# Kernel tuning notes

Hardware: AMD Instinct MI355X
Metric: run time of the kernel (lower is better)

Reference implementation:

```python
import jax, jax.numpy as jnp
import numpy as np

B = 512
NV = 6890   # SMPL vertices
NJ = 24     # SMPL joints
NB = 10     # shape betas
NP = 207    # pose blend coeffs = 23*9
# canonical SMPL kinematic tree: parent of joints 1..23
PARENT = np.array([0, 0, 0, 1, 2, 3, 4, 5, 6, 7, 8, 9, 9, 9, 12, 13, 14, 16, 17, 18, 19, 20, 21], dtype=np.int64)


def quat2mat(quat):
    # quat: [N,4] (w,x,y,z) -> [N,3,3]
    q = quat / jnp.linalg.norm(quat, axis=1, keepdims=True)
    w, x, y, z = q[:, 0], q[:, 1], q[:, 2], q[:, 3]
    w2, x2, y2, z2 = w * w, x * x, y * y, z * z
    wx, wy, wz = w * x, w * y, w * z
    xy, xz, yz = x * y, x * z, y * z
    rot = jnp.stack([
        w2 + x2 - y2 - z2, 2 * xy - 2 * wz, 2 * wy + 2 * xz,
        2 * wz + 2 * xy, w2 - x2 + y2 - z2, 2 * yz - 2 * wx,
        2 * xz - 2 * wy, 2 * wx + 2 * yz, w2 - x2 - y2 + z2], axis=1)
    return rot.reshape(-1, 3, 3)


def rodrigues(theta):
    # theta: [N,3] axis-angle -> [N,3,3]
    angle = jnp.linalg.norm(theta + 1e-8, axis=1, keepdims=True)
    normalized = theta / angle
    half = angle * 0.5
    quat = jnp.concatenate([jnp.cos(half), jnp.sin(half) * normalized], axis=1)
    return quat2mat(quat)


def setup_inputs() -> dict:
    key = jax.random.key(0)
    ks = jax.random.split(key, 8)
    pose = jax.random.normal(ks[0], (B, NJ * 3), dtype=jnp.float32) * 0.2
    beta = jax.random.normal(ks[1], (B, NB), dtype=jnp.float32)
    v_template = jax.random.normal(ks[2], (NV, 3), dtype=jnp.float32)
    shapedirs = jax.random.normal(ks[3], (NV, 3, NB), dtype=jnp.float32) * 0.01
    posedirs = jax.random.normal(ks[4], (NV, 3, NP), dtype=jnp.float32) * 0.01
    Jr = jax.random.uniform(ks[5], (NJ, NV), dtype=jnp.float32)
    J_regressor = Jr / jnp.sum(Jr, axis=1, keepdims=True)
    W = jax.random.uniform(ks[6], (NV, NJ), dtype=jnp.float32)
    weights = W / jnp.sum(W, axis=1, keepdims=True)
    return {"pose": pose, "beta": beta, "v_template": v_template,
            "shapedirs": shapedirs, "posedirs": posedirs,
            "J_regressor": J_regressor, "weights": weights,
            "parent": PARENT}


def reference(pose, beta, v_template, shapedirs, posedirs, J_regressor, weights, parent):
    dt = pose.dtype
    bsz = pose.shape[0]
    # shape blend: v_shaped [B,V,3]
    v_shaped = jnp.einsum('vdk,bk->bvd', shapedirs, beta) + v_template[None]
    J = jnp.einsum('jv,bvd->bjd', J_regressor, v_shaped)  # [B,24,3]
    # per-joint rotations from axis-angle
    R = rodrigues(pose.reshape(-1, 3)).reshape(bsz, NJ, 3, 3)
    # pose blend
    I3 = jnp.eye(3, dtype=dt)
    lrotmin = (R[:, 1:] - I3).reshape(bsz, NP)
    v_posed = v_shaped + jnp.einsum('vdp,bp->bvd', posedirs, lrotmin)
    # relative joint locations
    J_rel = jnp.concatenate([J[:, :1], J[:, 1:] - J[:, parent]], axis=1)
    # local 4x4 transforms G_local [B,24,4,4]
    bottom = jnp.broadcast_to(jnp.array([0., 0., 0., 1.], dtype=dt).reshape(1, 1, 1, 4), (bsz, NJ, 1, 4))
    G_local = jnp.concatenate([jnp.concatenate([R, J_rel[..., None]], axis=-1), bottom], axis=2)
    # forward kinematics along the tree (24 fixed steps)
    Gs = [G_local[:, 0]]
    for i in range(1, NJ):
        Gs.append(jnp.matmul(Gs[int(parent[i - 1])], G_local[:, i]))
    G = jnp.stack(Gs, axis=1)  # [B,24,4,4]
    # subtract rest-pose joint contribution from translation column
    J_h = jnp.concatenate([J, jnp.zeros((bsz, NJ, 1), dtype=dt)], axis=-1)  # [B,24,4]
    t_corr = jnp.einsum('bjmn,bjn->bjm', G, J_h)
    G = G.at[..., 3].add(-t_corr)
    # linear blend skinning
    T = jnp.einsum('vj,bjmn->bvmn', weights, G)  # [B,V,4,4]
    v_h = jnp.concatenate([v_posed, jnp.ones((bsz, NV, 1), dtype=dt)], axis=-1)
    v = jnp.einsum('bvmn,bvn->bvm', T, v_h)[..., :3]  # [B,V,3]
    return v
```

## Files before the change

kernel.cpp:

```cpp
#include <hip/hip_runtime.h>
#include <hip/hip_bf16.h>
#include <math.h>

#define NVERT 6890
#define NJN   24
#define NBETA 10
#define NPOSE 207
#define NBATCH 512
#define KDIM  224
#define NCOL  20670
#define NPAD  20736
#define VPAD  6912

typedef __attribute__((ext_vector_type(8))) short bh8;
typedef __attribute__((ext_vector_type(4))) float f4;

__device__ const int c_parent[23] = {0,0,0,1,2,3,4,5,6,7,8,9,9,9,12,13,14,16,17,18,19,20,21};


__global__ void k_prep(const float* __restrict__ pd, const float* __restrict__ sh,
                       const float* __restrict__ wts,
                       __hip_bfloat16* __restrict__ Bt, __hip_bfloat16* __restrict__ Wb) {
    const int btTotal = NPAD * KDIM;
    const int wbTotal = VPAD * 32;
    const int total = btTotal + wbTotal;
    for (int idx = blockIdx.x * blockDim.x + threadIdx.x; idx < total;
         idx += gridDim.x * blockDim.x) {
        if (idx < btTotal) {
            int col = idx / KDIM;
            int k = idx - col * KDIM;
            float val = 0.0f;
            if (col < NCOL) {
                int v = col / 3, d = col - v * 3;
                if (k < NPOSE)      val = pd[v * 621 + d * 207 + k];
                else if (k < 217)   val = sh[v * 30 + d * 10 + (k - 207)];
            }
            Bt[idx] = __float2bfloat16(val);
        } else {
            int r = idx - btTotal;
            int v = r >> 5, j = r & 31;
            float val = (v < NVERT && j < NJN) ? wts[v * NJN + j] : 0.0f;
            Wb[r] = __float2bfloat16(val);
        }
    }
}

__global__ void k_jreg(const float* __restrict__ Jr, const float* __restrict__ vt,
                       const float* __restrict__ sh, float* __restrict__ jb) {
    const int jd = blockIdx.x;
    const int j = jd / 3, d = jd % 3;
    float acc[11];
#pragma unroll
    for (int k = 0; k < 11; k++) acc[k] = 0.0f;
    for (int v = threadIdx.x; v < NVERT; v += 256) {
        float r = Jr[j * NVERT + v];
        acc[0] += r * vt[v * 3 + d];
        const float* sp = sh + v * 30 + d * 10;
#pragma unroll
        for (int k = 0; k < 10; k++) acc[1 + k] += r * sp[k];
    }
#pragma unroll
    for (int k = 0; k < 11; k++) {
#pragma unroll
        for (int off = 32; off > 0; off >>= 1)
            acc[k] += __shfl_down(acc[k], off);
    }
    __shared__ float red[4][11];
    const int lane = threadIdx.x & 63, wid = threadIdx.x >> 6;
    if (lane == 0) {
#pragma unroll
        for (int k = 0; k < 11; k++) red[wid][k] = acc[k];
    }
    __syncthreads();
    if (threadIdx.x == 0) {
#pragma unroll
        for (int k = 0; k < 11; k++) {
            float s = red[0][k] + red[1][k] + red[2][k] + red[3][k];
            if (k == 0) jb[jd] = s;
            else jb[72 + jd * 10 + (k - 1)] = s;
        }
    }
}

__global__ void k_pose(const float* __restrict__ pose, const float* __restrict__ beta,
                       const float* __restrict__ jb, __hip_bfloat16* __restrict__ A,
                       __hip_bfloat16* __restrict__ Gb) {
    const int b = blockIdx.x, t = threadIdx.x;
    __shared__ float sR[24][9], sJ[24][3], sGl[24][12], sG[24][12], sT[12][32];
    if (t < 24) {
        const float* th = pose + b * 72 + t * 3;
        float tx = th[0], ty = th[1], tz = th[2];
        float ax = tx + 1e-8f, ay = ty + 1e-8f, az = tz + 1e-8f;
        float ang = sqrtf(ax * ax + ay * ay + az * az);
        float inv = 1.0f / ang;
        float nx = tx * inv, ny = ty * inv, nz = tz * inv;
        float sw, cw;
        sincosf(0.5f * ang, &sw, &cw);
        float qw = cw, qx = sw * nx, qy = sw * ny, qz = sw * nz;
        float qn = 1.0f / sqrtf(qw * qw + qx * qx + qy * qy + qz * qz);
        qw *= qn; qx *= qn; qy *= qn; qz *= qn;
        float w2 = qw * qw, x2 = qx * qx, y2 = qy * qy, z2 = qz * qz;
        float wx = qw * qx, wy = qw * qy, wz = qw * qz;
        float xy = qx * qy, xz = qx * qz, yz = qy * qz;
        float R[9];
        R[0] = w2 + x2 - y2 - z2; R[1] = 2.f * (xy - wz); R[2] = 2.f * (wy + xz);
        R[3] = 2.f * (wz + xy);   R[4] = w2 - x2 + y2 - z2; R[5] = 2.f * (yz - wx);
        R[6] = 2.f * (xz - wy);   R[7] = 2.f * (wx + yz);   R[8] = w2 - x2 - y2 + z2;
#pragma unroll
        for (int k = 0; k < 9; k++) sR[t][k] = R[k];
        if (t >= 1) {
            __hip_bfloat16* ap = A + b * KDIM + (t - 1) * 9;
#pragma unroll
            for (int k = 0; k < 9; k++)
                ap[k] = __float2bfloat16(R[k] - ((k == 0 || k == 4 || k == 8) ? 1.f : 0.f));
        }
    }
    if (t < NBETA) A[b * KDIM + 207 + t] = __float2bfloat16(beta[b * NBETA + t]);
    if (t < 7)     A[b * KDIM + 217 + t] = __float2bfloat16(0.0f);
    if (t < 72) {
        const int j = t / 3;
        float Jv = jb[t];
        const float* c = jb + 72 + t * 10;
        const float* be = beta + b * NBETA;
#pragma unroll
        for (int k = 0; k < 10; k++) Jv += c[k] * be[k];
        sJ[j][t - j * 3] = Jv;
    }
    __syncthreads();
    if (t < 24) {
#pragma unroll
        for (int r = 0; r < 3; r++) {
            sGl[t][r * 4 + 0] = sR[t][r * 3 + 0];
            sGl[t][r * 4 + 1] = sR[t][r * 3 + 1];
            sGl[t][r * 4 + 2] = sR[t][r * 3 + 2];
            float jr = sJ[t][r];
            if (t > 0) jr -= sJ[c_parent[t - 1]][r];
            sGl[t][r * 4 + 3] = jr;
        }
    }
    __syncthreads();
    if (t < 12) sG[0][t] = sGl[0][t];
    __syncthreads();
    for (int i = 1; i < 24; i++) {
        if (t < 12) {
            const int m = t >> 2, n = t & 3;
            const int p = c_parent[i - 1];
            float val = sG[p][m * 4 + 0] * sGl[i][0 + n]
                      + sG[p][m * 4 + 1] * sGl[i][4 + n]
                      + sG[p][m * 4 + 2] * sGl[i][8 + n];
            if (n == 3) val += sG[p][m * 4 + 3];
            sG[i][t] = val;
        }
        __syncthreads();
    }
    if (t < 24) {
        float jx = sJ[t][0], jy = sJ[t][1], jz = sJ[t][2];
#pragma unroll
        for (int m = 0; m < 3; m++) {
            float g0 = sG[t][m * 4 + 0], g1 = sG[t][m * 4 + 1];
            float g2 = sG[t][m * 4 + 2], g3v = sG[t][m * 4 + 3];
            float tc = g0 * jx + g1 * jy + g2 * jz;
            sT[m * 4 + 0][t] = g0; sT[m * 4 + 1][t] = g1;
            sT[m * 4 + 2][t] = g2; sT[m * 4 + 3][t] = g3v - tc;
        }
    }
    __syncthreads();
    if (t < 16) {
        __hip_bfloat16* gbp = Gb + b * 512 + t * 32;
#pragma unroll
        for (int j = 0; j < 32; j++) {
            float v = (t < 12 && j < 24) ? sT[t][j] : 0.0f;
            gbp[j] = __float2bfloat16(v);
        }
    }
}

__global__ __launch_bounds__(256) void k_gemm(const __hip_bfloat16* __restrict__ A,
                                              const __hip_bfloat16* __restrict__ Bt,
                                              const float* __restrict__ vt,
                                              float* __restrict__ out) {
    const int lane = threadIdx.x & 63;
    const int wv = threadIdx.x >> 6;
    const int m0 = blockIdx.y * 32;
    const int n0 = blockIdx.x * 256 + wv * 64;
    const int l15 = lane & 15, lg = lane >> 4;

    const short* Ap = (const short*)A + (m0 + l15) * KDIM + lg * 8;
    const short* Bp = (const short*)Bt + (size_t)(n0 + l15) * KDIM + lg * 8;

    f4 acc[2][4];
#pragma unroll
    for (int mt = 0; mt < 2; mt++)
#pragma unroll
        for (int nr = 0; nr < 4; nr++) acc[mt][nr] = (f4){0.f, 0.f, 0.f, 0.f};

#pragma unroll
    for (int kk = 0; kk < 7; kk++) {
        bh8 a0 = *(const bh8*)(Ap + kk * 32);
        bh8 a1 = *(const bh8*)(Ap + 16 * KDIM + kk * 32);
#pragma unroll
        for (int nr = 0; nr < 4; nr++) {
            bh8 b = *(const bh8*)(Bp + (size_t)nr * 16 * KDIM + kk * 32);
            acc[0][nr] = __builtin_amdgcn_mfma_f32_16x16x32_bf16(a0, b, acc[0][nr], 0, 0, 0);
            acc[1][nr] = __builtin_amdgcn_mfma_f32_16x16x32_bf16(a1, b, acc[1][nr], 0, 0, 0);
        }
    }

#pragma unroll
    for (int mt = 0; mt < 2; mt++) {
#pragma unroll
        for (int nr = 0; nr < 4; nr++) {
            int col = n0 + nr * 16 + l15;
            if (col < NCOL) {
                float tv = vt[col];
                int rowb = m0 + mt * 16 + lg * 4;
#pragma unroll
                for (int r = 0; r < 4; r++)
                    out[(size_t)(rowb + r) * NCOL + col] = acc[mt][nr][r] + tv;
            }
        }
    }
}

__global__ __launch_bounds__(256) void k_lbs(const __hip_bfloat16* __restrict__ Gb,
                                             const __hip_bfloat16* __restrict__ Wb,
                                             float* __restrict__ out) {
    const int w = threadIdx.x >> 6, lane = threadIdx.x & 63;
    const int l15 = lane & 15, lg = lane >> 4;
    const int v = blockIdx.x * 64 + w * 16 + l15;
    const int b0 = blockIdx.y * 64;
    const bool vreal = (v < NVERT);
    const int vc = vreal ? v : (NVERT - 1);
    const bool doio = (lg < 3);

    bh8 wf = *(const bh8*)((const short*)Wb + v * 32 + lg * 8);

    for (int b = b0; b < b0 + 64; b++) {
        bh8 gf = *(const bh8*)((const short*)Gb + b * 512 + l15 * 32 + lg * 8);
        f4 T = __builtin_amdgcn_mfma_f32_16x16x32_bf16(gf, wf, (f4){0.f, 0.f, 0.f, 0.f}, 0, 0, 0);
        float x = 0.f, y = 0.f, z = 0.f;
        if (doio) {
            const float* ap = out + ((size_t)b * NVERT + vc) * 3;
            x = ap[0]; y = ap[1]; z = ap[2];
        }
        float val = T[0] * x + T[1] * y + T[2] * z + T[3];
        if (doio && vreal)
            out[((size_t)b * NVERT + v) * 3 + lg] = val;
    }
}

extern "C" void kernel_launch(void* const* d_in, const int* in_sizes, int n_in,
                              void* d_out, int out_size, void* d_ws, size_t ws_size,
                              hipStream_t stream) {
    const float* pose = (const float*)d_in[0];
    const float* beta = (const float*)d_in[1];
    const float* vtm  = (const float*)d_in[2];
    const float* sh   = (const float*)d_in[3];
    const float* pd   = (const float*)d_in[4];
    const float* Jr   = (const float*)d_in[5];
    const float* wts  = (const float*)d_in[6];
    float* out = (float*)d_out;

    __hip_bfloat16* Bt = (__hip_bfloat16*)d_ws;
    __hip_bfloat16* A  = Bt + (size_t)NPAD * KDIM;
    __hip_bfloat16* Gb = A + NBATCH * KDIM;
    __hip_bfloat16* Wb = Gb + NBATCH * 512;
    float* jb = (float*)(Wb + VPAD * 32);

    k_prep<<<2048, 256, 0, stream>>>(pd, sh, wts, Bt, Wb);
    k_jreg<<<72, 256, 0, stream>>>(Jr, vtm, sh, jb);
    k_pose<<<NBATCH, 128, 0, stream>>>(pose, beta, jb, A, Gb);
    k_gemm<<<dim3(81, 16), 256, 0, stream>>>(A, Bt, vtm, out);
    k_lbs<<<dim3(108, 8), 256, 0, stream>>>(Gb, Wb, out);
}
```

Measured before the change: 191.1 us.

## Merge weight prep with split-K joint regression and enlarge GEMM M-tile

The bf16 weight-conversion kernel and the joint-regressor kernel become one launch. The joint regression is split into 8 vertex chunks per output, combined with atomicAdd after a memset, so the 72-block reduction no longer runs serially with low parallelism. Each GEMM block now covers 128 batch rows instead of 32, reusing every B-fragment load across 8 M-tiles. This cuts redundant reads of the large posedirs matrix, at the cost of more accumulator registers, fewer blocks (324), and nondeterministic float atomics.

```diff
diff --git a/kernel.cpp b/kernel.cpp
--- a/kernel.cpp
+++ b/kernel.cpp
@@ -18,66 +18,68 @@
 __device__ const int c_parent[23] = {0,0,0,1,2,3,4,5,6,7,8,9,9,9,12,13,14,16,17,18,19,20,21};
 
 
-__global__ void k_prep(const float* __restrict__ pd, const float* __restrict__ sh,
-                       const float* __restrict__ wts,
-                       __hip_bfloat16* __restrict__ Bt, __hip_bfloat16* __restrict__ Wb) {
-    const int btTotal = NPAD * KDIM;
-    const int wbTotal = VPAD * 32;
-    const int total = btTotal + wbTotal;
-    for (int idx = blockIdx.x * blockDim.x + threadIdx.x; idx < total;
-         idx += gridDim.x * blockDim.x) {
-        if (idx < btTotal) {
-            int col = idx / KDIM;
-            int k = idx - col * KDIM;
-            float val = 0.0f;
-            if (col < NCOL) {
-                int v = col / 3, d = col - v * 3;
-                if (k < NPOSE)      val = pd[v * 621 + d * 207 + k];
-                else if (k < 217)   val = sh[v * 30 + d * 10 + (k - 207)];
+__global__ void k_setup(const float* __restrict__ pd, const float* __restrict__ sh,
+                        const float* __restrict__ wts, const float* __restrict__ Jr,
+                        const float* __restrict__ vt,
+                        __hip_bfloat16* __restrict__ Bt, __hip_bfloat16* __restrict__ Wb,
+                        float* __restrict__ jb) {
+    __shared__ float red[4][11];
+    if (blockIdx.x < 2048) {
+        const int btTotal = NPAD * KDIM;
+        const int total = btTotal + VPAD * 32;
+        for (int idx = blockIdx.x * 256 + threadIdx.x; idx < total; idx += 2048 * 256) {
+            if (idx < btTotal) {
+                int col = idx / KDIM;
+                int k = idx - col * KDIM;
+                float val = 0.0f;
+                if (col < NCOL) {
+                    int v = col / 3, d = col - v * 3;
+                    if (k < NPOSE)      val = pd[v * 621 + d * 207 + k];
+                    else if (k < 217)   val = sh[v * 30 + d * 10 + (k - 207)];
+                }
+                Bt[idx] = __float2bfloat16(val);
+            } else {
+                int r = idx - btTotal;
+                int v = r >> 5, j = r & 31;
+                float val = (v < NVERT && j < NJN) ? wts[v * NJN + j] : 0.0f;
+                Wb[r] = __float2bfloat16(val);
             }
-            Bt[idx] = __float2bfloat16(val);
-        } else {
-            int r = idx - btTotal;
-            int v = r >> 5, j = r & 31;
-            float val = (v < NVERT && j < NJN) ? wts[v * NJN + j] : 0.0f;
-            Wb[r] = __float2bfloat16(val);
-        }
-    }
-}
-
-__global__ void k_jreg(const float* __restrict__ Jr, const float* __restrict__ vt,
-                       const float* __restrict__ sh, float* __restrict__ jb) {
-    const int jd = blockIdx.x;
-    const int j = jd / 3, d = jd % 3;
-    float acc[11];
-#pragma unroll
-    for (int k = 0; k < 11; k++) acc[k] = 0.0f;
-    for (int v = threadIdx.x; v < NVERT; v += 256) {
-        float r = Jr[j * NVERT + v];
-        acc[0] += r * vt[v * 3 + d];
-        const float* sp = sh + v * 30 + d * 10;
-#pragma unroll
-        for (int k = 0; k < 10; k++) acc[1 + k] += r * sp[k];
-    }
-#pragma unroll
-    for (int k = 0; k < 11; k++) {
-#pragma unroll
-        for (int off = 32; off > 0; off >>= 1)
-            acc[k] += __shfl_down(acc[k], off);
-    }
-    __shared__ float red[4][11];
-    const int lane = threadIdx.x & 63, wid = threadIdx.x >> 6;
-    if (lane == 0) {
-#pragma unroll
-        for (int k = 0; k < 11; k++) red[wid][k] = acc[k];
-    }
-    __syncthreads();
-    if (threadIdx.x == 0) {
+        }
+    } else {
+        const int bid = blockIdx.x - 2048;
+        const int jd = bid % 72, chunk = bid / 72;
+        const int j = jd / 3, d = jd % 3;
+        const int vstart = chunk * 862;
+        int vend = vstart + 862; if (vend > NVERT) vend = NVERT;
+        float acc[11];
+#pragma unroll
+        for (int k = 0; k < 11; k++) acc[k] = 0.0f;
+        for (int v = vstart + threadIdx.x; v < vend; v += 256) {
+            float r = Jr[j * NVERT + v];
+            acc[0] += r * vt[v * 3 + d];
+            const float* sp = sh + v * 30 + d * 10;
+#pragma unroll
+            for (int k = 0; k < 10; k++) acc[1 + k] += r * sp[k];
+        }
 #pragma unroll
         for (int k = 0; k < 11; k++) {
-            float s = red[0][k] + red[1][k] + red[2][k] + red[3][k];
-            if (k == 0) jb[jd] = s;
-            else jb[72 + jd * 10 + (k - 1)] = s;
+#pragma unroll
+            for (int off = 32; off > 0; off >>= 1)
+                acc[k] += __shfl_down(acc[k], off);
+        }
+        const int lane = threadIdx.x & 63, wid = threadIdx.x >> 6;
+        if (lane == 0) {
+#pragma unroll
+            for (int k = 0; k < 11; k++) red[wid][k] = acc[k];
+        }
+        __syncthreads();
+        if (threadIdx.x == 0) {
+#pragma unroll
+            for (int k = 0; k < 11; k++) {
+                float s = red[0][k] + red[1][k] + red[2][k] + red[3][k];
+                if (k == 0) atomicAdd(&jb[jd], s);
+                else        atomicAdd(&jb[72 + jd * 10 + (k - 1)], s);
+            }
         }
     }
 }
@@ -181,38 +183,41 @@
                                               float* __restrict__ out) {
     const int lane = threadIdx.x & 63;
     const int wv = threadIdx.x >> 6;
-    const int m0 = blockIdx.y * 32;
+    const int m0 = blockIdx.y * 128;
     const int n0 = blockIdx.x * 256 + wv * 64;
     const int l15 = lane & 15, lg = lane >> 4;
 
     const short* Ap = (const short*)A + (m0 + l15) * KDIM + lg * 8;
     const short* Bp = (const short*)Bt + (size_t)(n0 + l15) * KDIM + lg * 8;
 
-    f4 acc[2][4];
-#pragma unroll
-    for (int mt = 0; mt < 2; mt++)
+    f4 acc[8][4];
+#pragma unroll
+    for (int mt = 0; mt < 8; mt++)
 #pragma unroll
         for (int nr = 0; nr < 4; nr++) acc[mt][nr] = (f4){0.f, 0.f, 0.f, 0.f};
 
 #pragma unroll
     for (int kk = 0; kk < 7; kk++) {
-        bh8 a0 = *(const bh8*)(Ap + kk * 32);
-        bh8 a1 = *(const bh8*)(Ap + 16 * KDIM + kk * 32);
+        bh8 a[8];
+#pragma unroll
+        for (int mt = 0; mt < 8; mt++)
+            a[mt] = *(const bh8*)(Ap + mt * 16 * KDIM + kk * 32);
 #pragma unroll
         for (int nr = 0; nr < 4; nr++) {
             bh8 b = *(const bh8*)(Bp + (size_t)nr * 16 * KDIM + kk * 32);
-            acc[0][nr] = __builtin_amdgcn_mfma_f32_16x16x32_bf16(a0, b, acc[0][nr], 0, 0, 0);
-            acc[1][nr] = __builtin_amdgcn_mfma_f32_16x16x32_bf16(a1, b, acc[1][nr], 0, 0, 0);
-        }
-    }
-
-#pragma unroll
-    for (int mt = 0; mt < 2; mt++) {
-#pragma unroll
-        for (int nr = 0; nr < 4; nr++) {
-            int col = n0 + nr * 16 + l15;
-            if (col < NCOL) {
-                float tv = vt[col];
+#pragma unroll
+            for (int mt = 0; mt < 8; mt++)
+                acc[mt][nr] = __builtin_amdgcn_mfma_f32_16x16x32_bf16(a[mt], b, acc[mt][nr], 0, 0, 0);
+        }
+    }
+
+#pragma unroll
+    for (int nr = 0; nr < 4; nr++) {
+        int col = n0 + nr * 16 + l15;
+        if (col < NCOL) {
+            float tv = vt[col];
+#pragma unroll
+            for (int mt = 0; mt < 8; mt++) {
                 int rowb = m0 + mt * 16 + lg * 4;
 #pragma unroll
                 for (int r = 0; r < 4; r++)
@@ -267,9 +272,9 @@
     __hip_bfloat16* Wb = Gb + NBATCH * 512;
     float* jb = (float*)(Wb + VPAD * 32);
 
-    k_prep<<<2048, 256, 0, stream>>>(pd, sh, wts, Bt, Wb);
-    k_jreg<<<72, 256, 0, stream>>>(Jr, vtm, sh, jb);
+    hipMemsetAsync(jb, 0, 792 * sizeof(float), stream);
+    k_setup<<<2624, 256, 0, stream>>>(pd, sh, wts, Jr, vtm, Bt, Wb, jb);
     k_pose<<<NBATCH, 128, 0, stream>>>(pose, beta, jb, A, Gb);
-    k_gemm<<<dim3(81, 16), 256, 0, stream>>>(A, Bt, vtm, out);
+    k_gemm<<<dim3(81, 4), 256, 0, stream>>>(A, Bt, vtm, out);
     k_lbs<<<dim3(108, 8), 256, 0, stream>>>(Gb, Wb, out);
 }
```

New measurement: 181.5 us. 5.0% less time.
